# Performance work log

Measured on AMD Instinct MI355X. Metric: run time of the kernel, lower is better.

Reference implementation:

```python
import jax, jax.numpy as jnp
import numpy as np

B, T, C, H = 4, 4096, 1024, 64

def setup_inputs() -> dict:
    key = jax.random.key(0)
    k1, k2, k3, k4, k5 = jax.random.split(key, 5)
    scale = 0.02
    return {
        "x": jax.random.normal(k1, (B, T, C), dtype=jnp.float32),
        "head_bias": jax.random.normal(k2, (T, T), dtype=jnp.float32) * 0.1,
        "w_k": jax.random.normal(k3, (C, H), dtype=jnp.float32) * scale,
        "w_q": jax.random.normal(k4, (C, H), dtype=jnp.float32) * scale,
        "w_v": jax.random.normal(k5, (C, H), dtype=jnp.float32) * scale,
    }

def reference(x, head_bias, w_k, w_q, w_v):
    # x: (B,T,C) ; projections: (B,T,H)
    k = jnp.einsum('btc,ch->bth', x, w_k)
    q = jnp.einsum('btc,ch->bth', x, w_q)
    v = jnp.einsum('btc,ch->bth', x, w_v)
    Tq = x.shape[1]
    # scores: (B,T,T) with RPE bias and causal mask
    scores = jnp.einsum('bqh,bkh->bqk', q, k) * (k.shape[-1] ** -0.5)
    scores = scores + head_bias[None, :, :]
    causal = jnp.tril(jnp.ones((Tq, Tq), dtype=bool))
    scores = jnp.where(causal[None, :, :], scores, -jnp.inf)
    weights = jax.nn.softmax(scores, axis=-1)
    out = jnp.einsum('bqk,bkh->bqh', weights, v)
    return out
```

## Files before the change

kernel.cpp:

```cpp
#include <hip/hip_runtime.h>
#include <hip/hip_bf16.h>


#define T_DIM 4096
#define C_DIM 1024
#define CK    256

typedef __attribute__((ext_vector_type(8))) short s16x8;
typedef __attribute__((ext_vector_type(4))) float f32x4;
typedef __attribute__((ext_vector_type(2))) unsigned int u32x2;

__device__ __forceinline__ short f2bf(float f) {
    unsigned u = __builtin_bit_cast(unsigned, f);
    u += 0x7FFFu + ((u >> 16) & 1u);
    return (short)(u >> 16);
}
__device__ __forceinline__ unsigned pack2(float a, float b) {
    unsigned ua = __builtin_bit_cast(unsigned, a);
    unsigned ub = __builtin_bit_cast(unsigned, b);
    ua += 0x7FFFu + ((ua >> 16) & 1u);
    ub += 0x7FFFu + ((ub >> 16) & 1u);
    return __builtin_amdgcn_perm(ub, ua, 0x07060302u);
}
__device__ __forceinline__ float bf2f(short s) {
    unsigned u = ((unsigned)(unsigned short)s) << 16;
    return __builtin_bit_cast(float, u);
}
__device__ __forceinline__ int chunk_off(int qt) {
    int g = qt >> 4, r = qt & 15;
    return qt + 8 * g * (g - 1) + r * g;
}

__global__ __launch_bounds__(256) void prep_frag(
    const float* __restrict__ wk, const float* __restrict__ wq,
    const float* __restrict__ wv, short* __restrict__ wfrag)
{
    int ksAll = blockIdx.x, mat = blockIdx.y;
    const float* w = (mat == 0) ? wk : ((mat == 1) ? wq : wv);
    float sc = (mat == 1) ? 0.125f : 1.0f;
    int nt = threadIdx.x >> 6, lane = threadIdx.x & 63;
    int quad = lane >> 4, l15 = lane & 15;
    int h = nt * 16 + l15;
    int cb = ksAll * 32 + quad * 8;
    s16x8 v;
    #pragma unroll
    for (int j = 0; j < 8; ++j) v[j] = f2bf(w[(cb + j) * 64 + h] * sc);
    *(s16x8*)&wfrag[((ksAll * 12 + mat * 4 + nt) * 64 + lane) * 8] = v;
}

union ProjSmem {
    short xs[32][1032];
    struct {
        short comb[2][16][136];
        short vsep[64][40];
    } c;
};

__global__ __launch_bounds__(256, 2) void proj_fused(
    const float* __restrict__ x, const short* __restrict__ wfrag,
    short* __restrict__ qb, short* __restrict__ kfrag, short* __restrict__ vfrag)
{
    __shared__ __align__(16) ProjSmem sm;

    int tid = threadIdx.x;
    int w = tid >> 6, lane = tid & 63;
    int rt = w >> 1, h = w & 1;
    int l15 = lane & 15, quad = lane >> 4;
    int m0 = blockIdx.x * 32;

    s16x8 fA[12], fB[12];
    {
        const s16x8* fb = (const s16x8*)&wfrag[((size_t)(h * 16) * 12 * 64 + lane) * 8];
        #pragma unroll
        for (int f = 0; f < 12; ++f) fA[f] = fb[f * 64];
    }

    #pragma unroll 8
    for (int p = 0; p < 32; ++p) {
        f32x4 v = *(const f32x4*)&x[(size_t)(m0 + p) * C_DIM + tid * 4];
        u32x2 d;
        d[0] = pack2(v[0], v[1]);
        d[1] = pack2(v[2], v[3]);
        *(u32x2*)&sm.xs[p][tid * 4] = d;
    }
    __syncthreads();

    f32x4 acc[12];
    #pragma unroll
    for (int i = 0; i < 12; ++i) acc[i] = (f32x4){0.f, 0.f, 0.f, 0.f};

    #pragma unroll 1
    for (int ks = 0; ks < 16; ks += 2) {
        {
            const s16x8* fb = (const s16x8*)&wfrag[((size_t)(h * 16 + ks + 1) * 12 * 64 + lane) * 8];
            #pragma unroll
            for (int f = 0; f < 12; ++f) fB[f] = fb[f * 64];
        }
        s16x8 af = *(const s16x8*)&sm.xs[rt * 16 + l15][(h * 16 + ks) * 32 + quad * 8];
        #pragma unroll
        for (int f = 0; f < 12; ++f)
            acc[f] = __builtin_amdgcn_mfma_f32_16x16x32_bf16(af, fA[f], acc[f], 0, 0, 0);
        if (ks + 2 < 16) {
            const s16x8* fb = (const s16x8*)&wfrag[((size_t)(h * 16 + ks + 2) * 12 * 64 + lane) * 8];
            #pragma unroll
            for (int f = 0; f < 12; ++f) fA[f] = fb[f * 64];
        }
        s16x8 af2 = *(const s16x8*)&sm.xs[rt * 16 + l15][(h * 16 + ks + 1) * 32 + quad * 8];
        #pragma unroll
        for (int f = 0; f < 12; ++f)
            acc[f] = __builtin_amdgcn_mfma_f32_16x16x32_bf16(af2, fB[f], acc[f], 0, 0, 0);
    }
    __syncthreads();

    if (h == 1) {
        #pragma unroll
        for (int f = 0; f < 8; ++f)
            #pragma unroll
            for (int r = 0; r < 4; ++r)
                sm.c.comb[rt][quad * 4 + r][(f >> 2) * 64 + (f & 3) * 16 + l15] = f2bf(acc[f][r]);
        #pragma unroll
        for (int f = 8; f < 12; ++f)
            #pragma unroll
            for (int r = 0; r < 4; ++r)
                sm.c.vsep[(f & 3) * 16 + l15][rt * 16 + quad * 4 + r] = f2bf(acc[f][r]);
    }
    __syncthreads();
    if (h == 0) {
        #pragma unroll
        for (int f = 0; f < 8; ++f)
            #pragma unroll
            for (int r = 0; r < 4; ++r) {
                int col = (f >> 2) * 64 + (f & 3) * 16 + l15, rr = quad * 4 + r;
                sm.c.comb[rt][rr][col] = f2bf(acc[f][r] + bf2f(sm.c.comb[rt][rr][col]));
            }
        #pragma unroll
        for (int f = 8; f < 12; ++f)
            #pragma unroll
            for (int r = 0; r < 4; ++r) {
                int hh = (f & 3) * 16 + l15, kk = rt * 16 + quad * 4 + r;
                sm.c.vsep[hh][kk] = f2bf(acc[f][r] + bf2f(sm.c.vsep[hh][kk]));
            }
    }
    __syncthreads();

    int b = m0 >> 12, t0 = m0 & 4095;
    int t016 = t0 >> 4, kt32 = t0 >> 5;
    {
        int row = tid >> 3, ch = tid & 7;
        s16x8 v = *(const s16x8*)&sm.c.comb[row >> 4][row & 15][64 + ch * 8];
        *(s16x8*)&qb[(size_t)(m0 + row) * 64 + ch * 8] = v;
    }
    {
        int kt = w & 1, ks = w >> 1;
        s16x8 v = *(const s16x8*)&sm.c.comb[kt][l15][ks * 32 + quad * 8];
        *(s16x8*)&kfrag[(size_t)(((b * 256 + t016 + kt) * 2 + ks) * 64 + lane) * 8] = v;
    }
    {
        int nt = w;
        s16x8 v = *(const s16x8*)&sm.c.vsep[nt * 16 + l15][quad * 8];
        *(s16x8*)&vfrag[(size_t)(((b * 128 + kt32) * 4 + nt) * 64 + lane) * 8] = v;
    }
}

#define LOADK(AK, k0) do {                                                    \
    int _kt16 = (k0) >> 4;                                                    \
    _Pragma("unroll")                                                         \
    for (int _n = 0; _n < 2; ++_n) {                                          \
        const short* _kp = kfb + (size_t)((_kt16 + _n) * 2) * 512 + lane * 8; \
        AK[_n * 2]     = *(const s16x8*)_kp;                                  \
        AK[_n * 2 + 1] = *(const s16x8*)(_kp + 512);                          \
    }                                                                         \
} while (0)

#define COMPUTEK(AK, k0) do {                                                 \
    int _kt32 = (k0) >> 5;                                                    \
    int _kl = (k0) - kstart;                                                  \
    s16x8 _bv[4];                                                             \
    _Pragma("unroll")                                                         \
    for (int _n = 0; _n < 4; ++_n)                                            \
        _bv[_n] = *(const s16x8*)(vfb + (size_t)(_kt32 * 4 + _n) * 512 + lane * 8); \
    f32x4 _aS[2];                                                             \
    _Pragma("unroll")                                                         \
    for (int _n = 0; _n < 2; ++_n) {                                          \
        _aS[_n] = (f32x4){0.f, 0.f, 0.f, 0.f};                                \
        _aS[_n] = __builtin_amdgcn_mfma_f32_16x16x32_bf16(AK[_n*2],   aq0, _aS[_n], 0, 0, 0); \
        _aS[_n] = __builtin_amdgcn_mfma_f32_16x16x32_bf16(AK[_n*2+1], aq1, _aS[_n], 0, 0, 0); \
    }                                                                         \
    _Pragma("unroll")                                                         \
    for (int _n = 0; _n < 2; ++_n) {                                          \
        f32x4 _vb = *(const f32x4*)&blds[l15][_kl + _n * 16 + quad * 4];      \
        float _sv[4];                                                         \
        _Pragma("unroll")                                                     \
        for (int _r = 0; _r < 4; ++_r) {                                      \
            _sv[_r] = _aS[_n][_r] + _vb[_r];                                  \
            if (mask_on && ((k0) + _n * 16 + quad * 4 + _r > strip0 + l15))   \
                _sv[_r] = -__builtin_inff();                                  \
            float _p = __expf(_sv[_r]);                                       \
            _sv[_r] = _p;                                                     \
            l_sum += _p;                                                      \
        }                                                                     \
        u32x2 _d;                                                             \
        _d[0] = pack2(_sv[0], _sv[1]);                                        \
        _d[1] = pack2(_sv[2], _sv[3]);                                        \
        *(u32x2*)&plds[w][l15][_n * 16 + quad * 4] = _d;                      \
    }                                                                         \
    s16x8 _ap = *(const s16x8*)&plds[w][l15][quad * 8];                       \
    _Pragma("unroll")                                                         \
    for (int _n = 0; _n < 4; ++_n)                                            \
        accO[_n] = __builtin_amdgcn_mfma_f32_16x16x32_bf16(_ap, _bv[_n], accO[_n], 0, 0, 0); \
} while (0)

__global__ __launch_bounds__(256, 4) void flash_part(
    const short* __restrict__ qb, const short* __restrict__ kfrag,
    const short* __restrict__ vfrag, const float* __restrict__ bias,
    short* __restrict__ po)
{
    int qt = blockIdx.x, c = blockIdx.y;
    if (c > (qt >> 4)) return;
    int q0 = qt * 16;
    int kstart = c * CK;
    int kend = min(kstart + CK, q0 + 16);

    __shared__ __align__(16) float blds[16][260];
    __shared__ __align__(16) short plds[4][16][40];

    int w = threadIdx.x >> 6, lane = threadIdx.x & 63;
    int b = w;
    int l15 = lane & 15, quad = lane >> 4;
    int strip0 = q0;

    #pragma unroll
    for (int p = 0; p < 4; ++p)
        *(f32x4*)&blds[p * 4 + w][lane * 4] =
            *(const f32x4*)&bias[(size_t)(q0 + p * 4 + w) * T_DIM + kstart + lane * 4];

    const short* qrow = qb + (size_t)(b * T_DIM + strip0 + l15) * 64;
    s16x8 aq0 = *(const s16x8*)(qrow + quad * 8);
    s16x8 aq1 = *(const s16x8*)(qrow + 32 + quad * 8);

    float l_sum = 0.f;
    f32x4 accO[4];
    #pragma unroll
    for (int nt = 0; nt < 4; ++nt) accO[nt] = (f32x4){0.f, 0.f, 0.f, 0.f};

    const short* kfb = kfrag + (size_t)b * 256 * 2 * 512;
    const short* vfb = vfrag + (size_t)b * 128 * 4 * 512;
    bool mask_on = (kend > strip0);

    __syncthreads();

    s16x8 akA[4], akB[4];
    int k0 = kstart;
    LOADK(akA, k0);
    while (true) {
        int k1 = k0 + 32;
        bool more = (k1 < kend);
        if (more) LOADK(akB, k1);
        COMPUTEK(akA, k0);
        if (!more) break;
        k0 = k1; k1 = k0 + 32;
        bool more2 = (k1 < kend);
        if (more2) LOADK(akA, k1);
        COMPUTEK(akB, k0);
        if (!more2) break;
        k0 = k1;
    }

    l_sum += __shfl_xor(l_sum, 16, 64);
    l_sum += __shfl_xor(l_sum, 32, 64);

    short* base = po + (size_t)((chunk_off(qt) + c) * 4 + b) * 1040;
    #pragma unroll
    for (int nt = 0; nt < 4; ++nt)
        #pragma unroll
        for (int r = 0; r < 4; ++r)
            base[(quad * 4 + r) * 64 + nt * 16 + l15] = f2bf(accO[nt][r]);
    if (quad == 0) base[1024 + l15] = f2bf(l_sum);
}

__global__ __launch_bounds__(256) void flash_reduce(
    const short* __restrict__ po, float* __restrict__ out)
{
    int idx = blockIdx.x * 256 + threadIdx.x;
    int row = idx >> 3, c8 = idx & 7;
    int b = row >> 12, t = row & 4095;
    int qt = t >> 4, rloc = t & 15;
    int nc = (t >> 8) + 1;
    int off = chunk_off(qt);
    float o[8];
    #pragma unroll
    for (int j = 0; j < 8; ++j) o[j] = 0.f;
    float l = 0.f;
    #pragma unroll 1
    for (int cc = 0; cc < nc; ++cc) {
        const short* base = po + (size_t)((off + cc) * 4 + b) * 1040;
        s16x8 v = *(const s16x8*)&base[rloc * 64 + c8 * 8];
        #pragma unroll
        for (int j = 0; j < 8; ++j) o[j] += bf2f(v[j]);
        l += bf2f(base[1024 + rloc]);
    }
    float inv = 1.0f / l;
    f32x4 r0 = (f32x4){o[0] * inv, o[1] * inv, o[2] * inv, o[3] * inv};
    f32x4 r1 = (f32x4){o[4] * inv, o[5] * inv, o[6] * inv, o[7] * inv};
    float* op = &out[(size_t)row * 64 + c8 * 8];
    *(f32x4*)op = r0;
    *(f32x4*)(op + 4) = r1;
}

extern "C" void kernel_launch(void* const* d_in, const int* in_sizes, int n_in,
                              void* d_out, int out_size, void* d_ws, size_t ws_size,
                              hipStream_t stream) {
    (void)in_sizes; (void)n_in; (void)out_size; (void)ws_size;
    const float* x    = (const float*)d_in[0];
    const float* bias = (const float*)d_in[1];
    const float* wk   = (const float*)d_in[2];
    const float* wq   = (const float*)d_in[3];
    const float* wv   = (const float*)d_in[4];
    float* out = (float*)d_out;

    short* wfrag = (short*)d_ws;
    short* qb    = wfrag + 196608;
    short* kfrag = qb + 1048576;
    short* vfrag = kfrag + 1048576;
    short* po    = vfrag + 1048576;

    prep_frag<<<dim3(32, 3), dim3(256), 0, stream>>>(wk, wq, wv, wfrag);
    proj_fused<<<dim3(512), dim3(256), 0, stream>>>(x, wfrag, qb, kfrag, vfrag);
    flash_part<<<dim3(256, 16), dim3(256), 0, stream>>>(qb, kfrag, vfrag, bias, po);
    flash_reduce<<<dim3(512), dim3(256), 0, stream>>>(po, out);
}
```

Baseline: 196.0 us.

## Use 32-row query tiles per block with bf16 bias staging and fragment-layout Q

The flash partial kernel now processes 32 query rows per block with 512 threads, two 16-row strips times four batches, so each bias tile is loaded once for twice as many rows. The bias is staged in LDS as packed bf16 instead of fp32, halving LDS use. Q is stored in MFMA fragment layout so it can be loaded directly, and the causal mask check is skipped for fully unmasked key blocks. The partial-output indexing and reduce kernel are updated for the new chunking. Rounding the bias to bf16 adds some error, and larger blocks change occupancy.

```diff
diff --git a/kernel.cpp b/kernel.cpp
--- a/kernel.cpp
+++ b/kernel.cpp
@@ -8,6 +8,7 @@
 
 typedef __attribute__((ext_vector_type(8))) short s16x8;
 typedef __attribute__((ext_vector_type(4))) float f32x4;
+typedef __attribute__((ext_vector_type(2))) float f32x2;
 typedef __attribute__((ext_vector_type(2))) unsigned int u32x2;
 
 __device__ __forceinline__ short f2bf(float f) {
@@ -27,8 +28,8 @@
     return __builtin_bit_cast(float, u);
 }
 __device__ __forceinline__ int chunk_off(int qt) {
-    int g = qt >> 4, r = qt & 15;
-    return qt + 8 * g * (g - 1) + r * g;
+    int g = qt >> 3, r = qt & 7;
+    return qt + 4 * g * (g - 1) + r * g;
 }
 
 __global__ __launch_bounds__(256) void prep_frag(
@@ -58,7 +59,7 @@
 
 __global__ __launch_bounds__(256, 2) void proj_fused(
     const float* __restrict__ x, const short* __restrict__ wfrag,
-    short* __restrict__ qb, short* __restrict__ kfrag, short* __restrict__ vfrag)
+    short* __restrict__ qfrag, short* __restrict__ kfrag, short* __restrict__ vfrag)
 {
     __shared__ __align__(16) ProjSmem sm;
 
@@ -146,14 +147,11 @@
     int b = m0 >> 12, t0 = m0 & 4095;
     int t016 = t0 >> 4, kt32 = t0 >> 5;
     {
-        int row = tid >> 3, ch = tid & 7;
-        s16x8 v = *(const s16x8*)&sm.c.comb[row >> 4][row & 15][64 + ch * 8];
-        *(s16x8*)&qb[(size_t)(m0 + row) * 64 + ch * 8] = v;
-    }
-    {
         int kt = w & 1, ks = w >> 1;
-        s16x8 v = *(const s16x8*)&sm.c.comb[kt][l15][ks * 32 + quad * 8];
-        *(s16x8*)&kfrag[(size_t)(((b * 256 + t016 + kt) * 2 + ks) * 64 + lane) * 8] = v;
+        s16x8 vk = *(const s16x8*)&sm.c.comb[kt][l15][ks * 32 + quad * 8];
+        *(s16x8*)&kfrag[(size_t)(((b * 256 + t016 + kt) * 2 + ks) * 64 + lane) * 8] = vk;
+        s16x8 vq = *(const s16x8*)&sm.c.comb[kt][l15][64 + ks * 32 + quad * 8];
+        *(s16x8*)&qfrag[(size_t)(((b * 256 + t016 + kt) * 2 + ks) * 64 + lane) * 8] = vq;
     }
     {
         int nt = w;
@@ -174,7 +172,6 @@
 
 #define COMPUTEK(AK, k0) do {                                                 \
     int _kt32 = (k0) >> 5;                                                    \
-    int _kl = (k0) - kstart;                                                  \
     s16x8 _bv[4];                                                             \
     _Pragma("unroll")                                                         \
     for (int _n = 0; _n < 4; ++_n)                                            \
@@ -186,22 +183,37 @@
         _aS[_n] = __builtin_amdgcn_mfma_f32_16x16x32_bf16(AK[_n*2],   aq0, _aS[_n], 0, 0, 0); \
         _aS[_n] = __builtin_amdgcn_mfma_f32_16x16x32_bf16(AK[_n*2+1], aq1, _aS[_n], 0, 0, 0); \
     }                                                                         \
+    float _sv[8];                                                             \
+    int _cb = ((k0) - kstart) >> 1;                                           \
     _Pragma("unroll")                                                         \
     for (int _n = 0; _n < 2; ++_n) {                                          \
-        f32x4 _vb = *(const f32x4*)&blds[l15][_kl + _n * 16 + quad * 4];      \
-        float _sv[4];                                                         \
+        u32x2 _bb = *(const u32x2*)&bldsu[(sl * 16 + l15) * 132 + _cb + _n * 8 + quad * 2]; \
+        _sv[_n*4+0] = _aS[_n][0] + __builtin_bit_cast(float, _bb[0] << 16);   \
+        _sv[_n*4+1] = _aS[_n][1] + __builtin_bit_cast(float, _bb[0] & 0xFFFF0000u); \
+        _sv[_n*4+2] = _aS[_n][2] + __builtin_bit_cast(float, _bb[1] << 16);   \
+        _sv[_n*4+3] = _aS[_n][3] + __builtin_bit_cast(float, _bb[1] & 0xFFFF0000u); \
+    }                                                                         \
+    if ((k0) + 31 > strip0) {                \
+        _Pragma("unroll")                                                     \
+        for (int _n = 0; _n < 2; ++_n) {                                      \
+            _Pragma("unroll")                                                 \
+            for (int _r = 0; _r < 4; ++_r) {                                  \
+                if ((k0) + _n * 16 + quad * 4 + _r > strip0 + l15)            \
+                    _sv[_n*4+_r] = -__builtin_inff();                         \
+            }                                                                 \
+        }                                                                     \
+    }                                                                         \
+    _Pragma("unroll")                                                         \
+    for (int _n = 0; _n < 2; ++_n) {                                          \
         _Pragma("unroll")                                                     \
         for (int _r = 0; _r < 4; ++_r) {                                      \
-            _sv[_r] = _aS[_n][_r] + _vb[_r];                                  \
-            if (mask_on && ((k0) + _n * 16 + quad * 4 + _r > strip0 + l15))   \
-                _sv[_r] = -__builtin_inff();                                  \
-            float _p = __expf(_sv[_r]);                                       \
-            _sv[_r] = _p;                                                     \
+            float _p = __expf(_sv[_n*4+_r]);                                  \
+            _sv[_n*4+_r] = _p;                                                \
             l_sum += _p;                                                      \
         }                                                                     \
         u32x2 _d;                                                             \
-        _d[0] = pack2(_sv[0], _sv[1]);                                        \
-        _d[1] = pack2(_sv[2], _sv[3]);                                        \
+        _d[0] = pack2(_sv[_n*4+0], _sv[_n*4+1]);                              \
+        _d[1] = pack2(_sv[_n*4+2], _sv[_n*4+3]);                              \
         *(u32x2*)&plds[w][l15][_n * 16 + quad * 4] = _d;                      \
     }                                                                         \
     s16x8 _ap = *(const s16x8*)&plds[w][l15][quad * 8];                       \
@@ -210,33 +222,38 @@
         accO[_n] = __builtin_amdgcn_mfma_f32_16x16x32_bf16(_ap, _bv[_n], accO[_n], 0, 0, 0); \
 } while (0)
 
-__global__ __launch_bounds__(256, 4) void flash_part(
-    const short* __restrict__ qb, const short* __restrict__ kfrag,
+__global__ __launch_bounds__(512, 6) void flash_part(
+    const short* __restrict__ qfrag, const short* __restrict__ kfrag,
     const short* __restrict__ vfrag, const float* __restrict__ bias,
     short* __restrict__ po)
 {
     int qt = blockIdx.x, c = blockIdx.y;
-    if (c > (qt >> 4)) return;
-    int q0 = qt * 16;
+    if (c > (qt >> 3)) return;
+    int q0 = qt * 32;
     int kstart = c * CK;
-    int kend = min(kstart + CK, q0 + 16);
-
-    __shared__ __align__(16) float blds[16][260];
-    __shared__ __align__(16) short plds[4][16][40];
-
-    int w = threadIdx.x >> 6, lane = threadIdx.x & 63;
-    int b = w;
+    int kend = min(kstart + CK, q0 + 32);
+
+    __shared__ unsigned bldsu[32 * 132];
+    __shared__ __align__(16) short plds[8][16][72];
+
+    int tid = threadIdx.x;
+    int w = tid >> 6, lane = tid & 63;
+    int b = w & 3, sl = w >> 2;
     int l15 = lane & 15, quad = lane >> 4;
-    int strip0 = q0;
-
-    #pragma unroll
-    for (int p = 0; p < 4; ++p)
-        *(f32x4*)&blds[p * 4 + w][lane * 4] =
-            *(const f32x4*)&bias[(size_t)(q0 + p * 4 + w) * T_DIM + kstart + lane * 4];
-
-    const short* qrow = qb + (size_t)(b * T_DIM + strip0 + l15) * 64;
-    s16x8 aq0 = *(const s16x8*)(qrow + quad * 8);
-    s16x8 aq1 = *(const s16x8*)(qrow + 32 + quad * 8);
+    int strip0 = q0 + sl * 16;
+
+    #pragma unroll
+    for (int p = 0; p < 8; ++p) {
+        int id = p * 512 + tid;
+        int row = id >> 7, col2 = id & 127;
+        f32x2 v = *(const f32x2*)&bias[(size_t)(q0 + row) * T_DIM + kstart + col2 * 2];
+        bldsu[row * 132 + col2] = pack2(v[0], v[1]);
+    }
+
+    int qt16 = strip0 >> 4;
+    const short* qfb = qfrag + (size_t)b * 256 * 2 * 512;
+    s16x8 aq0 = *(const s16x8*)(qfb + (size_t)(qt16 * 2) * 512 + lane * 8);
+    s16x8 aq1 = *(const s16x8*)(qfb + (size_t)(qt16 * 2 + 1) * 512 + lane * 8);
 
     float l_sum = 0.f;
     f32x4 accO[4];
@@ -245,7 +262,6 @@
 
     const short* kfb = kfrag + (size_t)b * 256 * 2 * 512;
     const short* vfb = vfrag + (size_t)b * 128 * 4 * 512;
-    bool mask_on = (kend > strip0);
 
     __syncthreads();
 
@@ -269,7 +285,7 @@
     l_sum += __shfl_xor(l_sum, 16, 64);
     l_sum += __shfl_xor(l_sum, 32, 64);
 
-    short* base = po + (size_t)((chunk_off(qt) + c) * 4 + b) * 1040;
+    short* base = po + (size_t)((chunk_off(qt) + c) * 8 + sl * 4 + b) * 1040;
     #pragma unroll
     for (int nt = 0; nt < 4; ++nt)
         #pragma unroll
@@ -284,7 +300,7 @@
     int idx = blockIdx.x * 256 + threadIdx.x;
     int row = idx >> 3, c8 = idx & 7;
     int b = row >> 12, t = row & 4095;
-    int qt = t >> 4, rloc = t & 15;
+    int qt = t >> 5, sl = (t >> 4) & 1, rloc = t & 15;
     int nc = (t >> 8) + 1;
     int off = chunk_off(qt);
     float o[8];
@@ -293,7 +309,7 @@
     float l = 0.f;
     #pragma unroll 1
     for (int cc = 0; cc < nc; ++cc) {
-        const short* base = po + (size_t)((off + cc) * 4 + b) * 1040;
+        const short* base = po + (size_t)((off + cc) * 8 + sl * 4 + b) * 1040;
         s16x8 v = *(const s16x8*)&base[rloc * 64 + c8 * 8];
         #pragma unroll
         for (int j = 0; j < 8; ++j) o[j] += bf2f(v[j]);
@@ -319,13 +335,13 @@
     float* out = (float*)d_out;
 
     short* wfrag = (short*)d_ws;
-    short* qb    = wfrag + 196608;
-    short* kfrag = qb + 1048576;
+    short* qfrag = wfrag + 196608;
+    short* kfrag = qfrag + 1048576;
     short* vfrag = kfrag + 1048576;
     short* po    = vfrag + 1048576;
 
     prep_frag<<<dim3(32, 3), dim3(256), 0, stream>>>(wk, wq, wv, wfrag);
-    proj_fused<<<dim3(512), dim3(256), 0, stream>>>(x, wfrag, qb, kfrag, vfrag);
-    flash_part<<<dim3(256, 16), dim3(256), 0, stream>>>(qb, kfrag, vfrag, bias, po);
+    proj_fused<<<dim3(512), dim3(256), 0, stream>>>(x, wfrag, qfrag, kfrag, vfrag);
+    flash_part<<<dim3(128, 16), dim3(512), 0, stream>>>(qfrag, kfrag, vfrag, bias, po);
     flash_reduce<<<dim3(512), dim3(256), 0, stream>>>(po, out);
 }
```

New measurement: 277.6 us. 1.42x slower.
